# Kernel tuning notes

Measured on AMD Instinct MI355X. Metric: run time of the kernel, lower is better.

## Reference

```python
import jax, jax.numpy as jnp
import numpy as np
import math

D = 2048
NH = 16
HD = D // NH
MULT = 4
EPS = 1e-6


def rmsnorm(x, g):
    norm = jax.lax.rsqrt(jnp.mean(x * x, axis=-1, keepdims=True) + EPS)
    return g * x * norm


def setup_inputs() -> dict:
    key = jax.random.key(0)
    ks = jax.random.split(key, 8)
    s = 0.02  # keep activations in a sane range
    return {
        "x": jax.random.normal(ks[0], (2, 2048, D), dtype=jnp.float32),
        "g1": jnp.ones((D,), dtype=jnp.float32),
        "wq": jax.random.normal(ks[1], (D, D), dtype=jnp.float32) * s,
        "wk": jax.random.normal(ks[2], (D, D), dtype=jnp.float32) * s,
        "wv": jax.random.normal(ks[3], (D, D), dtype=jnp.float32) * s,
        "wo": jax.random.normal(ks[4], (D, D), dtype=jnp.float32) * s,
        "g2": jnp.ones((D,), dtype=jnp.float32),
        "w_up": jax.random.normal(ks[5], (2 * D * MULT, D), dtype=jnp.float32) * s,
        "w_down": jax.random.normal(ks[6], (D, D * MULT), dtype=jnp.float32) * s,
    }


def reference(x, g1, wq, wk, wv, wo, g2, w_up, w_down):
    B, T, _ = x.shape
    # --- causal self-attention with pre-RMSNorm ---
    h = rmsnorm(x, g1)
    q = (h @ wq.T).reshape(B, T, NH, HD).transpose(0, 2, 1, 3)  # [B,H,T,hd]
    k = (h @ wk.T).reshape(B, T, NH, HD).transpose(0, 2, 1, 3)
    v = (h @ wv.T).reshape(B, T, NH, HD).transpose(0, 2, 1, 3)
    att = jnp.einsum("bhtd,bhsd->bhts", q, k) / math.sqrt(HD)  # [B,H,T,T]
    neg = jnp.finfo(att.dtype).min
    causal = jnp.triu(jnp.full((T, T), neg, dtype=att.dtype), k=1)
    att = att + causal
    w = jax.nn.softmax(att, axis=-1)
    z = jnp.einsum("bhts,bhsd->bhtd", w, v)  # [B,H,T,hd]
    z = z.transpose(0, 2, 1, 3).reshape(B, T, D)
    x = x + z @ wo.T
    # --- SwiGLU-style FFN (GELU gate) with pre-RMSNorm ---
    h2 = rmsnorm(x, g2)
    uv = h2 @ w_up.T  # [B,T,2*D*MULT]
    u, vgate = jnp.split(uv, 2, axis=-1)
    ff = (jax.nn.gelu(u, approximate=False) * vgate) @ w_down.T
    return x + ff
```

## Files before the change

kernel.cpp:

```cpp
#include <hip/hip_runtime.h>
#include <math.h>

typedef __bf16 bf16_t;
typedef __bf16 bf16x8 __attribute__((ext_vector_type(8)));
typedef __bf16 bf16x4 __attribute__((ext_vector_type(4)));
typedef float f32x4 __attribute__((ext_vector_type(4)));

#define D_MODEL 2048
#define N_HEADS 16
#define HEAD_D 128
#define SEQ 2048
#define NTOK 4096
#define DFF 8192
#define UPN 16384
#define PSTRIDE ((size_t)NTOK * D_MODEL)

#define GLDS16(g, l) __builtin_amdgcn_global_load_lds( \
    (const __attribute__((address_space(1))) void*)(g), \
    (__attribute__((address_space(3))) void*)(l), 16, 0, 0)

#define MFMA16(a, b, c) __builtin_amdgcn_mfma_f32_16x16x32_bf16((a), (b), (c), 0, 0, 0)

__device__ __forceinline__ void cvt_seg(const float* __restrict__ in,
                                        bf16_t* __restrict__ out, long n4) {
    long i = (long)blockIdx.x * 256 + threadIdx.x;
    long stride = (long)gridDim.x * 256;
    for (; i < n4; i += stride) {
        float4 f = ((const float4*)in)[i];
        bf16x4 v;
        v[0] = (bf16_t)f.x; v[1] = (bf16_t)f.y; v[2] = (bf16_t)f.z; v[3] = (bf16_t)f.w;
        ((bf16x4*)out)[i] = v;
    }
}
__global__ __launch_bounds__(256) void cvt6_kernel(
        const float* s0, bf16_t* d0, const float* s1, bf16_t* d1,
        const float* s2, bf16_t* d2, const float* s3, bf16_t* d3,
        const float* s4, bf16_t* d4, const float* s5, bf16_t* d5) {
    cvt_seg(s0, d0, (long)D_MODEL * D_MODEL / 4);
    cvt_seg(s1, d1, (long)D_MODEL * D_MODEL / 4);
    cvt_seg(s2, d2, (long)D_MODEL * D_MODEL / 4);
    cvt_seg(s3, d3, (long)D_MODEL * D_MODEL / 4);
    cvt_seg(s4, d4, (long)UPN * D_MODEL / 4);
    cvt_seg(s5, d5, (long)D_MODEL * DFF / 4);
}

__global__ __launch_bounds__(256) void rmsnorm_kernel(const float* __restrict__ x,
                                                      const float* __restrict__ g,
                                                      bf16_t* __restrict__ out) {
    int row = blockIdx.x;
    const float* xr = x + (size_t)row * D_MODEL;
    int c0 = threadIdx.x * 8;
    float4 a = *(const float4*)&xr[c0];
    float4 b = *(const float4*)&xr[c0 + 4];
    float ss = a.x*a.x + a.y*a.y + a.z*a.z + a.w*a.w
             + b.x*b.x + b.y*b.y + b.z*b.z + b.w*b.w;
    #pragma unroll
    for (int off = 1; off < 64; off <<= 1) ss += __shfl_xor(ss, off);
    __shared__ float red[4];
    if ((threadIdx.x & 63) == 0) red[threadIdx.x >> 6] = ss;
    __syncthreads();
    float norm = rsqrtf((red[0] + red[1] + red[2] + red[3]) * (1.f / D_MODEL) + 1e-6f);
    float4 ga = *(const float4*)&g[c0];
    float4 gb = *(const float4*)&g[c0 + 4];
    bf16x8 o;
    o[0] = (bf16_t)(a.x * ga.x * norm); o[1] = (bf16_t)(a.y * ga.y * norm);
    o[2] = (bf16_t)(a.z * ga.z * norm); o[3] = (bf16_t)(a.w * ga.w * norm);
    o[4] = (bf16_t)(b.x * gb.x * norm); o[5] = (bf16_t)(b.y * gb.y * norm);
    o[6] = (bf16_t)(b.z * gb.z * norm); o[7] = (bf16_t)(b.w * gb.w * norm);
    *(bf16x8*)&out[(size_t)row * D_MODEL + c0] = o;
}

__global__ __launch_bounds__(256) void combine3_kernel(const float* __restrict__ r,
        const bf16_t* __restrict__ p0, const bf16_t* __restrict__ p1,
        float* __restrict__ out, long n8) {
    long i = (long)blockIdx.x * 256 + threadIdx.x;
    long stride = (long)gridDim.x * 256;
    for (; i < n8; i += stride) {
        size_t e = (size_t)i * 8;
        float4 a0 = *(const float4*)&r[e];
        float4 a1 = *(const float4*)&r[e + 4];
        bf16x8 b0 = *(const bf16x8*)&p0[e];
        bf16x8 b1 = *(const bf16x8*)&p1[e];
        float4 o0, o1;
        o0.x = a0.x + (float)b0[0] + (float)b1[0];
        o0.y = a0.y + (float)b0[1] + (float)b1[1];
        o0.z = a0.z + (float)b0[2] + (float)b1[2];
        o0.w = a0.w + (float)b0[3] + (float)b1[3];
        o1.x = a1.x + (float)b0[4] + (float)b1[4];
        o1.y = a1.y + (float)b0[5] + (float)b1[5];
        o1.z = a1.z + (float)b0[6] + (float)b1[6];
        o1.w = a1.w + (float)b0[7] + (float)b1[7];
        *(float4*)&out[e] = o0;
        *(float4*)&out[e + 4] = o1;
    }
}

__global__ __launch_bounds__(256) void combine_rms_kernel(const float* __restrict__ r,
        const bf16_t* __restrict__ p0, const bf16_t* __restrict__ p1,
        const float* __restrict__ g, float* __restrict__ x1, bf16_t* __restrict__ h2) {
    int row = blockIdx.x;
    size_t rb = (size_t)row * D_MODEL;
    int c0 = threadIdx.x * 8;
    float4 a0 = *(const float4*)&r[rb + c0];
    float4 a1 = *(const float4*)&r[rb + c0 + 4];
    bf16x8 b0 = *(const bf16x8*)&p0[rb + c0];
    bf16x8 b1 = *(const bf16x8*)&p1[rb + c0];
    float v0 = a0.x + (float)b0[0] + (float)b1[0];
    float v1 = a0.y + (float)b0[1] + (float)b1[1];
    float v2 = a0.z + (float)b0[2] + (float)b1[2];
    float v3 = a0.w + (float)b0[3] + (float)b1[3];
    float v4 = a1.x + (float)b0[4] + (float)b1[4];
    float v5 = a1.y + (float)b0[5] + (float)b1[5];
    float v6 = a1.z + (float)b0[6] + (float)b1[6];
    float v7 = a1.w + (float)b0[7] + (float)b1[7];
    float4 w0; w0.x = v0; w0.y = v1; w0.z = v2; w0.w = v3;
    float4 w1; w1.x = v4; w1.y = v5; w1.z = v6; w1.w = v7;
    *(float4*)&x1[rb + c0] = w0;
    *(float4*)&x1[rb + c0 + 4] = w1;
    float ss = v0*v0 + v1*v1 + v2*v2 + v3*v3 + v4*v4 + v5*v5 + v6*v6 + v7*v7;
    #pragma unroll
    for (int off = 1; off < 64; off <<= 1) ss += __shfl_xor(ss, off);
    __shared__ float red[4];
    if ((threadIdx.x & 63) == 0) red[threadIdx.x >> 6] = ss;
    __syncthreads();
    float norm = rsqrtf((red[0] + red[1] + red[2] + red[3]) * (1.f / D_MODEL) + 1e-6f);
    float4 ga = *(const float4*)&g[c0];
    float4 gb = *(const float4*)&g[c0 + 4];
    bf16x8 o;
    o[0] = (bf16_t)(v0 * ga.x * norm); o[1] = (bf16_t)(v1 * ga.y * norm);
    o[2] = (bf16_t)(v2 * ga.z * norm); o[3] = (bf16_t)(v3 * ga.w * norm);
    o[4] = (bf16_t)(v4 * gb.x * norm); o[5] = (bf16_t)(v5 * gb.y * norm);
    o[6] = (bf16_t)(v6 * gb.z * norm); o[7] = (bf16_t)(v7 * gb.w * norm);
    *(bf16x8*)&h2[rb + c0] = o;
}

template<int MODE, int KSPLIT>
__global__ __launch_bounds__(512, 2)
void gemm256(const bf16_t* __restrict__ A, const bf16_t* __restrict__ W,
             void* __restrict__ o0, void* __restrict__ o1, void* __restrict__ o2,
             const float* __restrict__ res, int nbx, int K)
{
    __shared__ __align__(16) bf16_t ldsA[2 * 2 * 8192];
    __shared__ __align__(16) bf16_t ldsB[2 * 2 * 8192];
    const int tid = threadIdx.x;
    const int wave = tid >> 6, lane = tid & 63;
    const int lr = lane & 15, lg = lane >> 4;
    const int wm = wave >> 2, wn = wave & 3;

    const int nwg = gridDim.x, bid = blockIdx.x;
    const int cpx = nwg >> 3;
    const int s = (bid & 7) * cpx + (bid >> 3);
    const int by = s & 15, bx = s >> 4;
    const int bm0 = by * 256;
    const int bn0 = (MODE == 2) ? bx * 128 : bx * 256;
    const int z = (KSPLIT > 1) ? blockIdx.z : 0;
    const int Keff = K / KSPLIT, koff = z * Keff;

    const int rl = wave * 16 + (lane >> 2);
    const int gsw = ((lane & 3) ^ ((rl >> 1) & 3)) * 8;
    const bf16_t* asrc = A + (size_t)(bm0 + rl) * K + koff + gsw;
    const bf16_t* bsrc;
    size_t bstep2;
    if constexpr (MODE == 2) {
        int grp = rl >> 6, wi = rl & 63;
        int brow = (wi < 32) ? (bn0 + grp * 32 + wi) : (DFF + bn0 + grp * 32 + (wi - 32));
        bsrc = W + (size_t)brow * K + koff + gsw;
        bstep2 = (size_t)64 * K;
    } else {
        bsrc = W + (size_t)(bn0 + rl) * K + koff + gsw;
        bstep2 = (size_t)128 * K;
    }

    auto stA = [&](int t, int kh) {
        char* d = (char*)ldsA + (((t & 1) * 2 + kh) * 16384) + wave * 1024 + lane * 16;
        const bf16_t* sp = asrc + (size_t)t * 64 + kh * 32;
        GLDS16(sp, d);
        GLDS16(sp + (size_t)128 * K, d + 8192);
    };
    auto stB = [&](int t, int kh) {
        char* d = (char*)ldsB + (((t & 1) * 2 + kh) * 16384) + wave * 1024 + lane * 16;
        const bf16_t* sp = bsrc + (size_t)t * 64 + kh * 32;
        GLDS16(sp, d);
        GLDS16(sp + bstep2, d + 8192);
    };

    f32x4 acc[8][4] = {};
    const int xg = (lg ^ ((lr >> 1) & 3)) * 8;
    const int NKT = Keff >> 6;

    stA(0, 0); stB(0, 0); stA(0, 1); stB(0, 1); stA(1, 0); stB(1, 0);
    asm volatile("s_waitcnt vmcnt(8)" ::: "memory");
    __builtin_amdgcn_s_barrier();

#define TILE_BODY(T, S1, S2, W1, W2)                                                    \
    {                                                                                   \
        const int t_ = (T);                                                             \
        const bf16_t* Ab = ldsA + ((t_ & 1) * 2) * 8192;                                \
        const bf16_t* Bb = ldsB + ((t_ & 1) * 2) * 8192;                                \
        bf16x8 a0[4], a1[4], b0[4], b1[4];                                              \
                                                                      \
        _Pragma("unroll")                                                               \
        for (int i = 0; i < 4; ++i)                                                     \
            a0[i] = *(const bf16x8*)&Ab[(wm * 128 + i * 16 + lr) * 32 + xg];            \
        _Pragma("unroll")                                                               \
        for (int n = 0; n < 4; ++n)                                                     \
            b0[n] = *(const bf16x8*)&Bb[(wn * 64 + n * 16 + lr) * 32 + xg];             \
        if (S1) stA(t_ + 1, 1);                                                         \
        __builtin_amdgcn_s_setprio(1);                                                  \
        _Pragma("unroll")                                                               \
        for (int i = 0; i < 4; ++i)                                                     \
            _Pragma("unroll")                                                           \
            for (int n = 0; n < 4; ++n)                                                 \
                acc[i][n] = MFMA16(a0[i], b0[n], acc[i][n]);                            \
        __builtin_amdgcn_s_setprio(0);                                                  \
                                                                      \
        _Pragma("unroll")                                                               \
        for (int i = 0; i < 4; ++i)                                                     \
            a1[i] = *(const bf16x8*)&Ab[(wm * 128 + (i + 4) * 16 + lr) * 32 + xg];      \
        if (S1) stB(t_ + 1, 1);                                                         \
        __builtin_amdgcn_s_setprio(1);                                                  \
        _Pragma("unroll")                                                               \
        for (int i = 0; i < 4; ++i)                                                     \
            _Pragma("unroll")                                                           \
            for (int n = 0; n < 4; ++n)                                                 \
                acc[i + 4][n] = MFMA16(a1[i], b0[n], acc[i + 4][n]);                    \
        __builtin_amdgcn_s_setprio(0);                                                  \
        asm volatile("s_waitcnt vmcnt(" W1 ")" ::: "memory");                           \
        __builtin_amdgcn_s_barrier();                                                   \
                                                                      \
        _Pragma("unroll")                                                               \
        for (int i = 0; i < 4; ++i)                                                     \
            a0[i] = *(const bf16x8*)&Ab[8192 + (wm * 128 + i * 16 + lr) * 32 + xg];     \
        _Pragma("unroll")                                                               \
        for (int n = 0; n < 4; ++n)                                                     \
            b1[n] = *(const bf16x8*)&Bb[8192 + (wn * 64 + n * 16 + lr) * 32 + xg];      \
        if (S2) stA(t_ + 2, 0);                                                         \
        __builtin_amdgcn_s_setprio(1);                                                  \
        _Pragma("unroll")                                                               \
        for (int i = 0; i < 4; ++i)                                                     \
            _Pragma("unroll")                                                           \
            for (int n = 0; n < 4; ++n)                                                 \
                acc[i][n] = MFMA16(a0[i], b1[n], acc[i][n]);                            \
        __builtin_amdgcn_s_setprio(0);                                                  \
                                                                      \
        _Pragma("unroll")                                                               \
        for (int i = 0; i < 4; ++i)                                                     \
            a1[i] = *(const bf16x8*)&Ab[8192 + (wm * 128 + (i + 4) * 16 + lr) * 32 + xg]; \
        if (S2) stB(t_ + 2, 0);                                                         \
        __builtin_amdgcn_s_setprio(1);                                                  \
        _Pragma("unroll")                                                               \
        for (int i = 0; i < 4; ++i)                                                     \
            _Pragma("unroll")                                                           \
            for (int n = 0; n < 4; ++n)                                                 \
                acc[i + 4][n] = MFMA16(a1[i], b1[n], acc[i + 4][n]);                    \
        __builtin_amdgcn_s_setprio(0);                                                  \
        asm volatile("s_waitcnt vmcnt(" W2 ")" ::: "memory");                           \
        __builtin_amdgcn_s_barrier();                                                   \
    }

    for (int t = 0; t < NKT - 2; ++t) TILE_BODY(t, true, true, "8", "8");
    TILE_BODY(NKT - 2, true, false, "8", "4");
    TILE_BODY(NKT - 1, false, false, "0", "0");
#undef TILE_BODY

    if constexpr (MODE == 0) {
        const float qs = 0.08838834764831845f;
        const int th = bn0 >> 11;
        #pragma unroll
        for (int m = 0; m < 8; ++m) {
            int grow = bm0 + wm * 128 + m * 16 + lg * 4;
            #pragma unroll
            for (int n = 0; n < 4; ++n) {
                int gcol = bn0 + wn * 64 + n * 16 + lr;
                int c = gcol & 2047;
                if (th == 0) {
                    #pragma unroll
                    for (int r = 0; r < 4; ++r)
                        ((bf16_t*)o0)[(size_t)(grow + r) * D_MODEL + c] = (bf16_t)(acc[m][n][r] * qs);
                } else if (th == 1) {
                    #pragma unroll
                    for (int r = 0; r < 4; ++r)
                        ((bf16_t*)o1)[(size_t)(grow + r) * D_MODEL + c] = (bf16_t)acc[m][n][r];
                } else {
                    int hh = c >> 7, d = c & 127;
                    int bb = grow >> 11, t0 = grow & 2047;
                    bf16x4 st;
                    #pragma unroll
                    for (int r = 0; r < 4; ++r) st[r] = (bf16_t)acc[m][n][r];
                    *(bf16x4*)&((bf16_t*)o2)[((size_t)(bb * N_HEADS + hh) * HEAD_D + d) * SEQ + t0] = st;
                }
            }
        }
    } else if constexpr (MODE == 1) {
        bf16_t* po = (bf16_t*)o0 + (size_t)z * PSTRIDE;
        #pragma unroll
        for (int m = 0; m < 8; ++m) {
            int grow = bm0 + wm * 128 + m * 16 + lg * 4;
            #pragma unroll
            for (int n = 0; n < 4; ++n) {
                int gcol = bn0 + wn * 64 + n * 16 + lr;
                #pragma unroll
                for (int r = 0; r < 4; ++r) {
                    size_t idx = (size_t)(grow + r) * D_MODEL + gcol;
                    po[idx] = (bf16_t)acc[m][n][r];
                }
            }
        }
    } else {
        #pragma unroll
        for (int m = 0; m < 8; ++m) {
            int grow = bm0 + wm * 128 + m * 16 + lg * 4;
            #pragma unroll
            for (int n = 0; n < 2; ++n) {
                int gcol = bn0 + wn * 32 + n * 16 + lr;
                #pragma unroll
                for (int r = 0; r < 4; ++r) {
                    float u = acc[m][n][r], vg = acc[m][n + 2][r];
                    float ge = 0.5f * u * (1.f + erff(u * 0.70710678118654752f));
                    ((bf16_t*)o0)[(size_t)(grow + r) * DFF + gcol] = (bf16_t)(ge * vg);
                }
            }
        }
    }
}

#define SM_PV(svv, mr, lrr, oo)                                                         \
    {                                                                                   \
        float resc_[4]; bool dall_ = true;                                              \
        _Pragma("unroll")                                                               \
        for (int r = 0; r < 4; ++r) {                                                   \
            float mx = fmaxf(fmaxf(svv[0][r], svv[1][r]), fmaxf(svv[2][r], svv[3][r]));  \
            _Pragma("unroll")                                                           \
            for (int off = 1; off < 16; off <<= 1) mx = fmaxf(mx, __shfl_xor(mx, off)); \
            bool defer = __all(mx - mr[r] <= 8.f);                                      \
            float mnew = defer ? mr[r] : fmaxf(mr[r], mx);                              \
            resc_[r] = defer ? 1.f : __expf(mr[r] - mnew);                              \
            dall_ &= defer;                                                             \
            float sum = 0.f;                                                            \
            _Pragma("unroll")                                                           \
            for (int nb = 0; nb < 4; ++nb) {                                            \
                float p = __expf(svv[nb][r] - mnew);                                    \
                svv[nb][r] = p; sum += p;                                               \
            }                                                                           \
            _Pragma("unroll")                                                           \
            for (int off = 1; off < 16; off <<= 1) sum += __shfl_xor(sum, off);         \
            lrr[r] = lrr[r] * resc_[r] + sum; mr[r] = mnew;                             \
        }                                                                               \
        if (!dall_) {                                                                   \
            _Pragma("unroll")                                                           \
            for (int ob = 0; ob < 8; ++ob)                                              \
                _Pragma("unroll")                                                       \
                for (int r = 0; r < 4; ++r) oo[ob][r] *= resc_[r];                      \
        }                                                                               \
        _Pragma("unroll")                                                               \
        for (int nb = 0; nb < 4; ++nb)                                                  \
            _Pragma("unroll")                                                           \
            for (int r = 0; r < 4; ++r)                                                 \
                Ps[wave][(lg * 4 + r) * 72 + nb * 16 + lr] = (bf16_t)svv[nb][r];        \
        _Pragma("unroll")                                                               \
        for (int kk = 0; kk < 2; ++kk) {                                                \
            bf16x8 ap = *(const bf16x8*)&Ps[wave][lr * 72 + kk * 32 + lg * 8];          \
            _Pragma("unroll")                                                           \
            for (int ob = 0; ob < 8; ++ob) {                                            \
                bf16x8 bv = *(const bf16x8*)&Vts[(ob * 16 + lr) * 68 + kk * 32 + lg * 8]; \
                oo[ob] = MFMA16(ap, bv, oo[ob]);                                        \
            }                                                                           \
        }                                                                               \
    }

__global__ __launch_bounds__(256)
void attn_kernel(const bf16_t* __restrict__ Q, const bf16_t* __restrict__ K,
                 const bf16_t* __restrict__ Vt, bf16_t* __restrict__ Z)
{
    const int qb = blockIdx.z ? blockIdx.x : (gridDim.x - 1 - blockIdx.x);
    const int h = blockIdx.y, b = blockIdx.z;
    const int q0 = qb * 128;
    const int ktmax = 2 * qb + 1;
    const int tid = threadIdx.x, wave = tid >> 6, lane = tid & 63;
    const int lr = lane & 15, lg = lane >> 4;

    __shared__ __align__(16) bf16_t Qs[128 * 136];
    __shared__ __align__(16) bf16_t Ks[64 * 136];
    __shared__ __align__(16) bf16_t Vts[128 * 68];
    __shared__ __align__(16) bf16_t Ps[4][16 * 72];

    const size_t base = ((size_t)b * SEQ) * D_MODEL + (size_t)h * HEAD_D;
    const size_t vbase = (size_t)(b * N_HEADS + h) * HEAD_D * SEQ;

    const int kr = tid >> 4, kc = (tid & 15) * 8;
    const int vdr = tid >> 3, vc = (tid & 7) * 8;

    #pragma unroll
    for (int i = 0; i < 8; ++i)
        *(uint4*)&Qs[(kr + i * 16) * 136 + kc] =
            *(const uint4*)&Q[base + (size_t)(q0 + kr + i * 16) * D_MODEL + kc];

    uint4 k0g, k1g, k2g, k3g, v0g, v1g, v2g, v3g;
    const bf16_t* Kb = K + base + (size_t)kr * D_MODEL + kc;
    const bf16_t* Vb = Vt + vbase + (size_t)vdr * SEQ + vc;
    auto loadKV = [&](int kt) {
        const bf16_t* kp = Kb + (size_t)kt * 64 * D_MODEL;
        k0g = *(const uint4*)kp;
        k1g = *(const uint4*)(kp + (size_t)16 * D_MODEL);
        k2g = *(const uint4*)(kp + (size_t)32 * D_MODEL);
        k3g = *(const uint4*)(kp + (size_t)48 * D_MODEL);
        const bf16_t* vp = Vb + kt * 64;
        v0g = *(const uint4*)vp;
        v1g = *(const uint4*)(vp + (size_t)32 * SEQ);
        v2g = *(const uint4*)(vp + (size_t)64 * SEQ);
        v3g = *(const uint4*)(vp + (size_t)96 * SEQ);
    };
    loadKV(0);

    f32x4 oL[8] = {}, oH[8] = {};
    float mL[4], lL[4], mH[4], lH[4];
    #pragma unroll
    for (int r = 0; r < 4; ++r) { mL[r] = -1e30f; lL[r] = 0.f; mH[r] = -1e30f; lH[r] = 0.f; }

    for (int kt = 0; kt <= ktmax; ++kt) {
        __syncthreads();
        *(uint4*)&Ks[kr * 136 + kc] = k0g;
        *(uint4*)&Ks[(kr + 16) * 136 + kc] = k1g;
        *(uint4*)&Ks[(kr + 32) * 136 + kc] = k2g;
        *(uint4*)&Ks[(kr + 48) * 136 + kc] = k3g;
        *(uint4*)&Vts[vdr * 68 + vc] = v0g;
        *(uint4*)&Vts[(vdr + 32) * 68 + vc] = v1g;
        *(uint4*)&Vts[(vdr + 64) * 68 + vc] = v2g;
        *(uint4*)&Vts[(vdr + 96) * 68 + vc] = v3g;
        __syncthreads();
        if (kt < ktmax) loadKV(kt + 1);

        if (kt < ktmax) {
            f32x4 sv[4] = {};
            #pragma unroll
            for (int kk = 0; kk < 4; ++kk) {
                bf16x8 aq = *(const bf16x8*)&Qs[(wave * 16 + lr) * 136 + kk * 32 + lg * 8];
                #pragma unroll
                for (int nb = 0; nb < 4; ++nb) {
                    bf16x8 bk = *(const bf16x8*)&Ks[(nb * 16 + lr) * 136 + kk * 32 + lg * 8];
                    sv[nb] = MFMA16(aq, bk, sv[nb]);
                }
            }
            if (kt == ktmax - 1) {
                #pragma unroll
                for (int nb = 0; nb < 4; ++nb)
                    #pragma unroll
                    for (int r = 0; r < 4; ++r) {
                        int qrel = 16 * wave + lg * 4 + r;
                        int krel = nb * 16 + lr;
                        if (krel > qrel) sv[nb][r] = -1e30f;
                    }
            }
            SM_PV(sv, mL, lL, oL)
        }
        {
            f32x4 sv[4] = {};
            #pragma unroll
            for (int kk = 0; kk < 4; ++kk) {
                bf16x8 aq = *(const bf16x8*)&Qs[(64 + wave * 16 + lr) * 136 + kk * 32 + lg * 8];
                #pragma unroll
                for (int nb = 0; nb < 4; ++nb) {
                    bf16x8 bk = *(const bf16x8*)&Ks[(nb * 16 + lr) * 136 + kk * 32 + lg * 8];
                    sv[nb] = MFMA16(aq, bk, sv[nb]);
                }
            }
            if (kt == ktmax) {
                #pragma unroll
                for (int nb = 0; nb < 4; ++nb)
                    #pragma unroll
                    for (int r = 0; r < 4; ++r) {
                        int qrel = 16 * wave + lg * 4 + r;
                        int krel = nb * 16 + lr;
                        if (krel > qrel) sv[nb][r] = -1e30f;
                    }
            }
            SM_PV(sv, mH, lH, oH)
        }
    }
    #pragma unroll
    for (int r = 0; r < 4; ++r) { lL[r] = 1.f / lL[r]; lH[r] = 1.f / lH[r]; }
    #pragma unroll
    for (int ob = 0; ob < 8; ++ob)
        #pragma unroll
        for (int r = 0; r < 4; ++r) {
            int t = q0 + 16 * wave + lg * 4 + r;
            Z[base + (size_t)t * D_MODEL + ob * 16 + lr] = (bf16_t)(oL[ob][r] * lL[r]);
            Z[base + (size_t)(t + 64) * D_MODEL + ob * 16 + lr] = (bf16_t)(oH[ob][r] * lH[r]);
        }
}
#undef SM_PV

extern "C" void kernel_launch(void* const* d_in, const int* in_sizes, int n_in,
                              void* d_out, int out_size, void* d_ws, size_t ws_size,
                              hipStream_t stream)
{
    const float* x   = (const float*)d_in[0];
    const float* g1  = (const float*)d_in[1];
    const float* wq  = (const float*)d_in[2];
    const float* wk  = (const float*)d_in[3];
    const float* wv  = (const float*)d_in[4];
    const float* wo  = (const float*)d_in[5];
    const float* g2  = (const float*)d_in[6];
    const float* wup = (const float*)d_in[7];
    const float* wdn = (const float*)d_in[8];
    float* out = (float*)d_out;

    char* wsp = (char*)d_ws;
    size_t off = 0;
    auto alloc = [&](size_t bytes) { void* p = wsp + off; off += (bytes + 255) & ~255ull; return p; };
    bf16_t* wq_b  = (bf16_t*)alloc((size_t)D_MODEL * D_MODEL * 2);
    bf16_t* wk_b  = (bf16_t*)alloc((size_t)D_MODEL * D_MODEL * 2);
    bf16_t* wv_b  = (bf16_t*)alloc((size_t)D_MODEL * D_MODEL * 2);
    bf16_t* wo_b  = (bf16_t*)alloc((size_t)D_MODEL * D_MODEL * 2);
    bf16_t* wup_b = (bf16_t*)alloc((size_t)UPN * D_MODEL * 2);
    bf16_t* wdn_b = (bf16_t*)alloc((size_t)D_MODEL * DFF * 2);
    bf16_t* h_b   = (bf16_t*)alloc((size_t)NTOK * D_MODEL * 2);
    bf16_t* q_b   = (bf16_t*)alloc((size_t)NTOK * D_MODEL * 2);
    bf16_t* k_b   = (bf16_t*)alloc((size_t)NTOK * D_MODEL * 2);
    bf16_t* vt_b  = (bf16_t*)alloc((size_t)NTOK * D_MODEL * 2);
    bf16_t* z_b   = (bf16_t*)alloc((size_t)NTOK * D_MODEL * 2);
    float*  x1    = (float*) alloc((size_t)NTOK * D_MODEL * 4);
    bf16_t* h2_b  = (bf16_t*)alloc((size_t)NTOK * D_MODEL * 2);
    bf16_t* act_b = (bf16_t*)alloc((size_t)NTOK * DFF * 2);
    bf16_t* pbuf = h_b;

    cvt6_kernel<<<2048, 256, 0, stream>>>(wq, wq_b, wk, wk_b, wv, wv_b,
                                          wo, wo_b, wup, wup_b, wdn, wdn_b);

    rmsnorm_kernel<<<NTOK, 256, 0, stream>>>(x, g1, h_b);

    gemm256<0, 1><<<24 * 16, 512, 0, stream>>>(h_b, wq_b, q_b, k_b, vt_b, nullptr, 24, D_MODEL);

    attn_kernel<<<dim3(SEQ / 128, N_HEADS, 2), 256, 0, stream>>>(q_b, k_b, vt_b, z_b);

    gemm256<1, 2><<<dim3(8 * 16, 1, 2), 512, 0, stream>>>(z_b, wo_b, pbuf, nullptr, nullptr, nullptr, 8, D_MODEL);
    combine_rms_kernel<<<NTOK, 256, 0, stream>>>(x, pbuf, pbuf + PSTRIDE, g2, x1, h2_b);

    gemm256<2, 1><<<64 * 16, 512, 0, stream>>>(h2_b, wup_b, act_b, nullptr, nullptr, nullptr, 64, D_MODEL);

    gemm256<1, 2><<<dim3(8 * 16, 1, 2), 512, 0, stream>>>(act_b, wdn_b, pbuf, nullptr, nullptr, nullptr, 8, DFF);
    combine3_kernel<<<2048, 256, 0, stream>>>(x1, pbuf, pbuf + PSTRIDE, out,
                                              (long)NTOK * D_MODEL / 8);
}
```

Measured before the change: 877.9 us.

## Use dedicated 128x256-tile QKV GEMM and raise MFMA priority in attention

Replaces the 256x256-tile QKV projection with a dedicated kernel using 128-row tiles, giving 768 workgroups instead of 384 so the wave count fills the GPU's compute units better. The new kernel keeps the same double-buffered LDS pipeline and epilogue (Q scaling, K store, V transposed store). Separately, the attention kernel's QK and PV MFMA loops are wrapped in s_setprio raises. Smaller tiles mean less operand reuse per workgroup and more global traffic.

Result: no change. 882.5 us (+0.5%).

```diff
diff --git a/kernel.cpp b/kernel.cpp
--- a/kernel.cpp
+++ b/kernel.cpp
@@ -137,8 +137,7 @@
 template<int MODE, int KSPLIT>
 __global__ __launch_bounds__(512, 2)
 void gemm256(const bf16_t* __restrict__ A, const bf16_t* __restrict__ W,
-             void* __restrict__ o0, void* __restrict__ o1, void* __restrict__ o2,
-             const float* __restrict__ res, int nbx, int K)
+             void* __restrict__ o0, const float* __restrict__ res, int nbx, int K)
 {
     __shared__ __align__(16) bf16_t ldsA[2 * 2 * 8192];
     __shared__ __align__(16) bf16_t ldsB[2 * 2 * 8192];
@@ -198,7 +197,6 @@
         const bf16_t* Ab = ldsA + ((t_ & 1) * 2) * 8192;                                \
         const bf16_t* Bb = ldsB + ((t_ & 1) * 2) * 8192;                                \
         bf16x8 a0[4], a1[4], b0[4], b1[4];                                              \
-                                                                      \
         _Pragma("unroll")                                                               \
         for (int i = 0; i < 4; ++i)                                                     \
             a0[i] = *(const bf16x8*)&Ab[(wm * 128 + i * 16 + lr) * 32 + xg];            \
@@ -213,7 +211,6 @@
             for (int n = 0; n < 4; ++n)                                                 \
                 acc[i][n] = MFMA16(a0[i], b0[n], acc[i][n]);                            \
         __builtin_amdgcn_s_setprio(0);                                                  \
-                                                                      \
         _Pragma("unroll")                                                               \
         for (int i = 0; i < 4; ++i)                                                     \
             a1[i] = *(const bf16x8*)&Ab[(wm * 128 + (i + 4) * 16 + lr) * 32 + xg];      \
@@ -227,7 +224,6 @@
         __builtin_amdgcn_s_setprio(0);                                                  \
         asm volatile("s_waitcnt vmcnt(" W1 ")" ::: "memory");                           \
         __builtin_amdgcn_s_barrier();                                                   \
-                                                                      \
         _Pragma("unroll")                                                               \
         for (int i = 0; i < 4; ++i)                                                     \
             a0[i] = *(const bf16x8*)&Ab[8192 + (wm * 128 + i * 16 + lr) * 32 + xg];     \
@@ -242,7 +238,6 @@
             for (int n = 0; n < 4; ++n)                                                 \
                 acc[i][n] = MFMA16(a0[i], b1[n], acc[i][n]);                            \
         __builtin_amdgcn_s_setprio(0);                                                  \
-                                                                      \
         _Pragma("unroll")                                                               \
         for (int i = 0; i < 4; ++i)                                                     \
             a1[i] = *(const bf16x8*)&Ab[8192 + (wm * 128 + (i + 4) * 16 + lr) * 32 + xg]; \
@@ -263,35 +258,7 @@
     TILE_BODY(NKT - 1, false, false, "0", "0");
 #undef TILE_BODY
 
-    if constexpr (MODE == 0) {
-        const float qs = 0.08838834764831845f;
-        const int th = bn0 >> 11;
-        #pragma unroll
-        for (int m = 0; m < 8; ++m) {
-            int grow = bm0 + wm * 128 + m * 16 + lg * 4;
-            #pragma unroll
-            for (int n = 0; n < 4; ++n) {
-                int gcol = bn0 + wn * 64 + n * 16 + lr;
-                int c = gcol & 2047;
-                if (th == 0) {
-                    #pragma unroll
-                    for (int r = 0; r < 4; ++r)
-                        ((bf16_t*)o0)[(size_t)(grow + r) * D_MODEL + c] = (bf16_t)(acc[m][n][r] * qs);
-                } else if (th == 1) {
-                    #pragma unroll
-                    for (int r = 0; r < 4; ++r)
-                        ((bf16_t*)o1)[(size_t)(grow + r) * D_MODEL + c] = (bf16_t)acc[m][n][r];
-                } else {
-                    int hh = c >> 7, d = c & 127;
-                    int bb = grow >> 11, t0 = grow & 2047;
-                    bf16x4 st;
-                    #pragma unroll
-                    for (int r = 0; r < 4; ++r) st[r] = (bf16_t)acc[m][n][r];
-                    *(bf16x4*)&((bf16_t*)o2)[((size_t)(bb * N_HEADS + hh) * HEAD_D + d) * SEQ + t0] = st;
-                }
-            }
-        }
-    } else if constexpr (MODE == 1) {
+    if constexpr (MODE == 1) {
         bf16_t* po = (bf16_t*)o0 + (size_t)z * PSTRIDE;
         #pragma unroll
         for (int m = 0; m < 8; ++m) {
@@ -324,6 +291,123 @@
     }
 }
 
+__global__ __launch_bounds__(512, 2)
+void gemm_qkv(const bf16_t* __restrict__ A, const bf16_t* __restrict__ W,
+              bf16_t* __restrict__ qo, bf16_t* __restrict__ ko, bf16_t* __restrict__ vo,
+              int K)
+{
+    __shared__ __align__(16) bf16_t ldsA[2 * 2 * 4096];
+    __shared__ __align__(16) bf16_t ldsB[2 * 2 * 8192];
+    const int tid = threadIdx.x;
+    const int wave = tid >> 6, lane = tid & 63;
+    const int lr = lane & 15, lg = lane >> 4;
+    const int wm = wave >> 2, wn = wave & 3;
+
+    const int bid = blockIdx.x;
+    const int s = (bid & 7) * 96 + (bid >> 3);
+    const int by = s & 31, bx = s >> 5;
+    const int bm0 = by * 128, bn0 = bx * 256;
+
+    const int rl = wave * 16 + (lane >> 2);
+    const int gsw = ((lane & 3) ^ ((rl >> 1) & 3)) * 8;
+    const bf16_t* asrc = A + (size_t)(bm0 + rl) * K + gsw;
+    const bf16_t* bsrc = W + (size_t)(bn0 + rl) * K + gsw;
+
+    auto stA = [&](int t, int kh) {
+        char* d = (char*)ldsA + (((t & 1) * 2 + kh) * 8192) + wave * 1024 + lane * 16;
+        GLDS16(asrc + (size_t)t * 64 + kh * 32, d);
+    };
+    auto stB = [&](int t, int kh) {
+        char* d = (char*)ldsB + (((t & 1) * 2 + kh) * 16384) + wave * 1024 + lane * 16;
+        const bf16_t* sp = bsrc + (size_t)t * 64 + kh * 32;
+        GLDS16(sp, d);
+        GLDS16(sp + (size_t)128 * K, d + 8192);
+    };
+
+    f32x4 acc[4][4] = {};
+    const int xg = (lg ^ ((lr >> 1) & 3)) * 8;
+    const int NKT = K >> 6;
+
+    stA(0, 0); stB(0, 0); stA(0, 1); stB(0, 1); stA(1, 0); stB(1, 0);
+    asm volatile("s_waitcnt vmcnt(6)" ::: "memory");
+    __builtin_amdgcn_s_barrier();
+
+#define QKV_TILE(T, S1, S2, W1, W2)                                                     \
+    {                                                                                   \
+        const int t_ = (T);                                                             \
+        const bf16_t* Ab = ldsA + ((t_ & 1) * 2) * 4096;                                \
+        const bf16_t* Bb = ldsB + ((t_ & 1) * 2) * 8192;                                \
+        bf16x8 af[4], bfr[4];                                                           \
+                                                                           \
+        _Pragma("unroll")                                                               \
+        for (int i = 0; i < 4; ++i)                                                     \
+            af[i] = *(const bf16x8*)&Ab[(wm * 64 + i * 16 + lr) * 32 + xg];             \
+        _Pragma("unroll")                                                               \
+        for (int n = 0; n < 4; ++n)                                                     \
+            bfr[n] = *(const bf16x8*)&Bb[(wn * 64 + n * 16 + lr) * 32 + xg];            \
+        if (S1) { stA(t_ + 1, 1); stB(t_ + 1, 1); }                                     \
+        __builtin_amdgcn_s_setprio(1);                                                  \
+        _Pragma("unroll")                                                               \
+        for (int i = 0; i < 4; ++i)                                                     \
+            _Pragma("unroll")                                                           \
+            for (int n = 0; n < 4; ++n)                                                 \
+                acc[i][n] = MFMA16(af[i], bfr[n], acc[i][n]);                           \
+        __builtin_amdgcn_s_setprio(0);                                                  \
+        asm volatile("s_waitcnt vmcnt(" W1 ")" ::: "memory");                           \
+        __builtin_amdgcn_s_barrier();                                                   \
+                                                                           \
+        _Pragma("unroll")                                                               \
+        for (int i = 0; i < 4; ++i)                                                     \
+            af[i] = *(const bf16x8*)&Ab[4096 + (wm * 64 + i * 16 + lr) * 32 + xg];      \
+        _Pragma("unroll")                                                               \
+        for (int n = 0; n < 4; ++n)                                                     \
+            bfr[n] = *(const bf16x8*)&Bb[8192 + (wn * 64 + n * 16 + lr) * 32 + xg];     \
+        if (S2) { stA(t_ + 2, 0); stB(t_ + 2, 0); }                                     \
+        __builtin_amdgcn_s_setprio(1);                                                  \
+        _Pragma("unroll")                                                               \
+        for (int i = 0; i < 4; ++i)                                                     \
+            _Pragma("unroll")                                                           \
+            for (int n = 0; n < 4; ++n)                                                 \
+                acc[i][n] = MFMA16(af[i], bfr[n], acc[i][n]);                           \
+        __builtin_amdgcn_s_setprio(0);                                                  \
+        asm volatile("s_waitcnt vmcnt(" W2 ")" ::: "memory");                           \
+        __builtin_amdgcn_s_barrier();                                                   \
+    }
+
+    for (int t = 0; t < NKT - 2; ++t) QKV_TILE(t, true, true, "6", "6");
+    QKV_TILE(NKT - 2, true, false, "6", "3");
+    QKV_TILE(NKT - 1, false, false, "0", "0");
+#undef QKV_TILE
+
+    const float qs = 0.08838834764831845f;
+    const int th = bn0 >> 11;
+    #pragma unroll
+    for (int m = 0; m < 4; ++m) {
+        int grow = bm0 + wm * 64 + m * 16 + lg * 4;
+        #pragma unroll
+        for (int n = 0; n < 4; ++n) {
+            int gcol = bn0 + wn * 64 + n * 16 + lr;
+            int c = gcol & 2047;
+            if (th == 0) {
+                #pragma unroll
+                for (int r = 0; r < 4; ++r)
+                    qo[(size_t)(grow + r) * D_MODEL + c] = (bf16_t)(acc[m][n][r] * qs);
+            } else if (th == 1) {
+                #pragma unroll
+                for (int r = 0; r < 4; ++r)
+                    ko[(size_t)(grow + r) * D_MODEL + c] = (bf16_t)acc[m][n][r];
+            } else {
+                int hh = c >> 7, d = c & 127;
+                int bb = grow >> 11, t0 = grow & 2047;
+                bf16x4 st;
+                #pragma unroll
+                for (int r = 0; r < 4; ++r) st[r] = (bf16_t)acc[m][n][r];
+                *(bf16x4*)&vo[((size_t)(bb * N_HEADS + hh) * HEAD_D + d) * SEQ + t0] = st;
+            }
+        }
+    }
+}
+
 #define SM_PV(svv, mr, lrr, oo)                                                         \
     {                                                                                   \
         float resc_[4]; bool dall_ = true;                                              \
@@ -357,6 +441,7 @@
             _Pragma("unroll")                                                           \
             for (int r = 0; r < 4; ++r)                                                 \
                 Ps[wave][(lg * 4 + r) * 72 + nb * 16 + lr] = (bf16_t)svv[nb][r];        \
+        __builtin_amdgcn_s_setprio(1);                                                  \
         _Pragma("unroll")                                                               \
         for (int kk = 0; kk < 2; ++kk) {                                                \
             bf16x8 ap = *(const bf16x8*)&Ps[wave][lr * 72 + kk * 32 + lg * 8];          \
@@ -366,6 +451,7 @@
                 oo[ob] = MFMA16(ap, bv, oo[ob]);                                        \
             }                                                                           \
         }                                                                               \
+        __builtin_amdgcn_s_setprio(0);                                                  \
     }
 
 __global__ __launch_bounds__(256)
@@ -432,6 +518,7 @@
 
         if (kt < ktmax) {
             f32x4 sv[4] = {};
+            __builtin_amdgcn_s_setprio(1);
             #pragma unroll
             for (int kk = 0; kk < 4; ++kk) {
                 bf16x8 aq = *(const bf16x8*)&Qs[(wave * 16 + lr) * 136 + kk * 32 + lg * 8];
@@ -441,6 +528,7 @@
                     sv[nb] = MFMA16(aq, bk, sv[nb]);
                 }
             }
+            __builtin_amdgcn_s_setprio(0);
             if (kt == ktmax - 1) {
                 #pragma unroll
                 for (int nb = 0; nb < 4; ++nb)
@@ -455,6 +543,7 @@
         }
         {
             f32x4 sv[4] = {};
+            __builtin_amdgcn_s_setprio(1);
             #pragma unroll
             for (int kk = 0; kk < 4; ++kk) {
                 bf16x8 aq = *(const bf16x8*)&Qs[(64 + wave * 16 + lr) * 136 + kk * 32 + lg * 8];
@@ -464,6 +553,7 @@
                     sv[nb] = MFMA16(aq, bk, sv[nb]);
                 }
             }
+            __builtin_amdgcn_s_setprio(0);
             if (kt == ktmax) {
                 #pragma unroll
                 for (int nb = 0; nb < 4; ++nb)
@@ -529,16 +619,16 @@
 
     rmsnorm_kernel<<<NTOK, 256, 0, stream>>>(x, g1, h_b);
 
-    gemm256<0, 1><<<24 * 16, 512, 0, stream>>>(h_b, wq_b, q_b, k_b, vt_b, nullptr, 24, D_MODEL);
+    gemm_qkv<<<768, 512, 0, stream>>>(h_b, wq_b, q_b, k_b, vt_b, D_MODEL);
 
     attn_kernel<<<dim3(SEQ / 128, N_HEADS, 2), 256, 0, stream>>>(q_b, k_b, vt_b, z_b);
 
-    gemm256<1, 2><<<dim3(8 * 16, 1, 2), 512, 0, stream>>>(z_b, wo_b, pbuf, nullptr, nullptr, nullptr, 8, D_MODEL);
+    gemm256<1, 2><<<dim3(8 * 16, 1, 2), 512, 0, stream>>>(z_b, wo_b, pbuf, nullptr, 8, D_MODEL);
     combine_rms_kernel<<<NTOK, 256, 0, stream>>>(x, pbuf, pbuf + PSTRIDE, g2, x1, h2_b);
 
-    gemm256<2, 1><<<64 * 16, 512, 0, stream>>>(h2_b, wup_b, act_b, nullptr, nullptr, nullptr, 64, D_MODEL);
-
-    gemm256<1, 2><<<dim3(8 * 16, 1, 2), 512, 0, stream>>>(act_b, wdn_b, pbuf, nullptr, nullptr, nullptr, 8, DFF);
+    gemm256<2, 1><<<64 * 16, 512, 0, stream>>>(h2_b, wup_b, act_b, nullptr, 64, D_MODEL);
+
+    gemm256<1, 2><<<dim3(8 * 16, 1, 2), 512, 0, stream>>>(act_b, wdn_b, pbuf, nullptr, 8, DFF);
     combine3_kernel<<<2048, 256, 0, stream>>>(x1, pbuf, pbuf + PSTRIDE, out,
                                               (long)NTOK * D_MODEL / 8);
 }
```

## Replace up/gate GEMM with simpler 128x64 tiled kernel

Applied to the files above, without the earlier changes.

The fused up-projection + GELU-gate GEMM moves off the heavily pipelined 256x256 double-buffered kernel onto a new 128-row by 64-output tile kernel with 256 threads. That kernel uses single-buffered 32-wide K steps and two barriers per step. The intent is likely better occupancy or load balance with many more small blocks. The cost is lower data reuse per tile, no overlap of global loads with MFMA work, and more barrier overhead. The old MODE 2 paths in gemm256 are removed.

New measurement: 996.3 us. 13.5% more time.

```diff
diff --git a/kernel.cpp b/kernel.cpp
--- a/kernel.cpp
+++ b/kernel.cpp
@@ -134,6 +134,79 @@
     *(bf16x8*)&h2[rb + c0] = o;
 }
 
+__global__ __launch_bounds__(256)
+void gemm128_upgate(const bf16_t* __restrict__ A, const bf16_t* __restrict__ W,
+                    bf16_t* __restrict__ act)
+{
+    __shared__ __align__(16) bf16_t As[128 * 32];
+    __shared__ __align__(16) bf16_t Bs[128 * 32];
+    const int tid = threadIdx.x;
+    const int wave = tid >> 6, lane = tid & 63;
+    const int lr = lane & 15, lg = lane >> 4;
+    const int wm = wave >> 1, wn = wave & 1;
+
+    const int bid = blockIdx.x;
+    const int s = (bid & 7) * 512 + (bid >> 3);
+    const int by = s & 31, bx = s >> 5;
+    const int bm0 = by * 128, bn0 = bx * 64;
+
+    const int rl = tid >> 2;
+    const int gsw = ((tid & 3) ^ ((rl >> 1) & 3)) * 8;
+    const bf16_t* asrc0 = A + (size_t)(bm0 + rl) * D_MODEL + gsw;
+    const bf16_t* asrc1 = asrc0 + (size_t)64 * D_MODEL;
+    const bf16_t* busrc = W + (size_t)(bn0 + rl) * D_MODEL + gsw;
+    const bf16_t* bvsrc = W + (size_t)(DFF + bn0 + rl) * D_MODEL + gsw;
+    char* const adst0 = (char*)As + tid * 16;
+    char* const adst1 = (char*)As + 4096 + tid * 16;
+    char* const budst = (char*)Bs + tid * 16;
+    char* const bvdst = (char*)Bs + 4096 + tid * 16;
+
+    f32x4 acc[4][4] = {};
+    const int xg = (lg ^ ((lr >> 1) & 3)) * 8;
+
+    for (int k0 = 0; k0 < D_MODEL; k0 += 32) {
+        __syncthreads();
+        GLDS16(asrc0 + k0, adst0);
+        GLDS16(asrc1 + k0, adst1);
+        GLDS16(busrc + k0, budst);
+        GLDS16(bvsrc + k0, bvdst);
+        __syncthreads();
+        bf16x8 af[4], bu[2], bv[2];
+        #pragma unroll
+        for (int m = 0; m < 4; ++m)
+            af[m] = *(const bf16x8*)&As[(wm * 64 + m * 16 + lr) * 32 + xg];
+        #pragma unroll
+        for (int n = 0; n < 2; ++n) {
+            bu[n] = *(const bf16x8*)&Bs[(wn * 32 + n * 16 + lr) * 32 + xg];
+            bv[n] = *(const bf16x8*)&Bs[(64 + wn * 32 + n * 16 + lr) * 32 + xg];
+        }
+        __builtin_amdgcn_s_setprio(1);
+        #pragma unroll
+        for (int m = 0; m < 4; ++m) {
+            acc[m][0] = MFMA16(af[m], bu[0], acc[m][0]);
+            acc[m][1] = MFMA16(af[m], bu[1], acc[m][1]);
+            acc[m][2] = MFMA16(af[m], bv[0], acc[m][2]);
+            acc[m][3] = MFMA16(af[m], bv[1], acc[m][3]);
+        }
+        __builtin_amdgcn_s_setprio(0);
+    }
+
+    #pragma unroll
+    for (int m = 0; m < 4; ++m) {
+        int grow = bm0 + wm * 64 + m * 16 + lg * 4;
+        #pragma unroll
+        for (int n = 0; n < 2; ++n) {
+            int gcol = bn0 + wn * 32 + n * 16 + lr;
+            #pragma unroll
+            for (int r = 0; r < 4; ++r) {
+                float u = acc[m][n][r], vg = acc[m][n + 2][r];
+                float ge = 0.5f * u * (1.f + erff(u * 0.70710678118654752f));
+                act[(size_t)(grow + r) * DFF + gcol] = (bf16_t)(ge * vg);
+            }
+        }
+    }
+}
+
 template<int MODE, int KSPLIT>
 __global__ __launch_bounds__(512, 2)
 void gemm256(const bf16_t* __restrict__ A, const bf16_t* __restrict__ W,
@@ -152,24 +225,15 @@
     const int s = (bid & 7) * cpx + (bid >> 3);
     const int by = s & 15, bx = s >> 4;
     const int bm0 = by * 256;
-    const int bn0 = (MODE == 2) ? bx * 128 : bx * 256;
+    const int bn0 = bx * 256;
     const int z = (KSPLIT > 1) ? blockIdx.z : 0;
     const int Keff = K / KSPLIT, koff = z * Keff;
 
     const int rl = wave * 16 + (lane >> 2);
     const int gsw = ((lane & 3) ^ ((rl >> 1) & 3)) * 8;
     const bf16_t* asrc = A + (size_t)(bm0 + rl) * K + koff + gsw;
-    const bf16_t* bsrc;
-    size_t bstep2;
-    if constexpr (MODE == 2) {
-        int grp = rl >> 6, wi = rl & 63;
-        int brow = (wi < 32) ? (bn0 + grp * 32 + wi) : (DFF + bn0 + grp * 32 + (wi - 32));
-        bsrc = W + (size_t)brow * K + koff + gsw;
-        bstep2 = (size_t)64 * K;
-    } else {
-        bsrc = W + (size_t)(bn0 + rl) * K + koff + gsw;
-        bstep2 = (size_t)128 * K;
-    }
+    const bf16_t* bsrc = W + (size_t)(bn0 + rl) * K + koff + gsw;
+    const size_t bstep2 = (size_t)128 * K;
 
     auto stA = [&](int t, int kh) {
         char* d = (char*)ldsA + (((t & 1) * 2 + kh) * 16384) + wave * 1024 + lane * 16;
@@ -198,7 +262,6 @@
         const bf16_t* Ab = ldsA + ((t_ & 1) * 2) * 8192;                                \
         const bf16_t* Bb = ldsB + ((t_ & 1) * 2) * 8192;                                \
         bf16x8 a0[4], a1[4], b0[4], b1[4];                                              \
-                                                                      \
         _Pragma("unroll")                                                               \
         for (int i = 0; i < 4; ++i)                                                     \
             a0[i] = *(const bf16x8*)&Ab[(wm * 128 + i * 16 + lr) * 32 + xg];            \
@@ -213,7 +276,6 @@
             for (int n = 0; n < 4; ++n)                                                 \
                 acc[i][n] = MFMA16(a0[i], b0[n], acc[i][n]);                            \
         __builtin_amdgcn_s_setprio(0);                                                  \
-                                                                      \
         _Pragma("unroll")                                                               \
         for (int i = 0; i < 4; ++i)                                                     \
             a1[i] = *(const bf16x8*)&Ab[(wm * 128 + (i + 4) * 16 + lr) * 32 + xg];      \
@@ -227,7 +289,6 @@
         __builtin_amdgcn_s_setprio(0);                                                  \
         asm volatile("s_waitcnt vmcnt(" W1 ")" ::: "memory");                           \
         __builtin_amdgcn_s_barrier();                                                   \
-                                                                      \
         _Pragma("unroll")                                                               \
         for (int i = 0; i < 4; ++i)                                                     \
             a0[i] = *(const bf16x8*)&Ab[8192 + (wm * 128 + i * 16 + lr) * 32 + xg];     \
@@ -242,7 +303,6 @@
             for (int n = 0; n < 4; ++n)                                                 \
                 acc[i][n] = MFMA16(a0[i], b1[n], acc[i][n]);                            \
         __builtin_amdgcn_s_setprio(0);                                                  \
-                                                                      \
         _Pragma("unroll")                                                               \
         for (int i = 0; i < 4; ++i)                                                     \
             a1[i] = *(const bf16x8*)&Ab[8192 + (wm * 128 + (i + 4) * 16 + lr) * 32 + xg]; \
@@ -291,7 +351,7 @@
                 }
             }
         }
-    } else if constexpr (MODE == 1) {
+    } else {
         bf16_t* po = (bf16_t*)o0 + (size_t)z * PSTRIDE;
         #pragma unroll
         for (int m = 0; m < 8; ++m) {
@@ -303,21 +363,6 @@
                 for (int r = 0; r < 4; ++r) {
                     size_t idx = (size_t)(grow + r) * D_MODEL + gcol;
                     po[idx] = (bf16_t)acc[m][n][r];
-                }
-            }
-        }
-    } else {
-        #pragma unroll
-        for (int m = 0; m < 8; ++m) {
-            int grow = bm0 + wm * 128 + m * 16 + lg * 4;
-            #pragma unroll
-            for (int n = 0; n < 2; ++n) {
-                int gcol = bn0 + wn * 32 + n * 16 + lr;
-                #pragma unroll
-                for (int r = 0; r < 4; ++r) {
-                    float u = acc[m][n][r], vg = acc[m][n + 2][r];
-                    float ge = 0.5f * u * (1.f + erff(u * 0.70710678118654752f));
-                    ((bf16_t*)o0)[(size_t)(grow + r) * DFF + gcol] = (bf16_t)(ge * vg);
                 }
             }
         }
@@ -536,7 +581,7 @@
     gemm256<1, 2><<<dim3(8 * 16, 1, 2), 512, 0, stream>>>(z_b, wo_b, pbuf, nullptr, nullptr, nullptr, 8, D_MODEL);
     combine_rms_kernel<<<NTOK, 256, 0, stream>>>(x, pbuf, pbuf + PSTRIDE, g2, x1, h2_b);
 
-    gemm256<2, 1><<<64 * 16, 512, 0, stream>>>(h2_b, wup_b, act_b, nullptr, nullptr, nullptr, 64, D_MODEL);
+    gemm128_upgate<<<4096, 256, 0, stream>>>(h2_b, wup_b, act_b);
 
     gemm256<1, 2><<<dim3(8 * 16, 1, 2), 512, 0, stream>>>(act_b, wdn_b, pbuf, nullptr, nullptr, nullptr, 8, DFF);
     combine3_kernel<<<2048, 256, 0, stream>>>(x1, pbuf, pbuf + PSTRIDE, out,
```
